# Optimization experiments

Measured on AMD Instinct MI355X. Metric: run time of the kernel, lower is better.

## Reference

```python
import jax, jax.numpy as jnp
import numpy as np


def setup_inputs() -> dict:
    key = jax.random.key(0)
    kx, ka = jax.random.split(key)
    B, N, D = 8, 4096, 32
    x = jax.random.normal(kx, (B, N, D), dtype=jnp.float32)
    # adjacency-like nonnegative weights (dense branch of GsumLayer)
    a = jax.random.uniform(ka, (B, N, N), dtype=jnp.float32)
    return {"x": x, "a": a}


def reference(x, a):
    # GsumLayer dense branch: out[b] = a[b] @ x[b]  -> [B, N, D]
    return jnp.einsum('bnm,bmd->bnd', a, x)
```

## Files before the change

### kernel.cpp

```cpp
#include <hip/hip_runtime.h>


#define GN 4096
#define GD 32
#define GB 8
#define BKC 256
#define NCH (GN / BKC)
#define NT 512
#define NW 8
#define TILE_N 128

typedef float f32x4 __attribute__((ext_vector_type(4)));
typedef short s16x8 __attribute__((ext_vector_type(8)));

__global__ __launch_bounds__(256, 4) void xprep(
    const float* __restrict__ x,
    unsigned short* __restrict__ xth,
    unsigned short* __restrict__ xtl)
{
    const int t  = threadIdx.x;
    const int b  = blockIdx.x >> 5;
    const int kc = blockIdx.x & 31;
    const int d  = t & 31;
    const int kb = t >> 5;
    const int k0 = kc * 128 + kb * 16;
    const float* xb = x + (long long)b * GN * GD;

    __attribute__((aligned(16))) unsigned short hi[16];
    __attribute__((aligned(16))) unsigned short lo[16];
    #pragma unroll
    for (int j = 0; j < 16; ++j) {
        float f = xb[(long long)(k0 + j) * GD + d];
        unsigned u  = __float_as_uint(f);
        unsigned hb = (u + 0x8000u) >> 16;
        float hif   = __uint_as_float(hb << 16);
        hi[j] = (unsigned short)hb;
        lo[j] = (unsigned short)((__float_as_uint(f - hif) + 0x8000u) >> 16);
    }
    long long ob = ((long long)(b * GD + d)) * GN + k0;
    *(s16x8*)(xth + ob)     = *(const s16x8*)&hi[0];
    *(s16x8*)(xth + ob + 8) = *(const s16x8*)&hi[8];
    *(s16x8*)(xtl + ob)     = *(const s16x8*)&lo[0];
    *(s16x8*)(xtl + ob + 8) = *(const s16x8*)&lo[8];
}

__global__ __launch_bounds__(NT, 2) void gsum_mfma(
    const float* __restrict__ a,
    const unsigned short* __restrict__ xth,
    const unsigned short* __restrict__ xtl,
    float* __restrict__ out)
{
    __shared__ float As[NW][16][BKC];

    const int t  = threadIdx.x;
    const int w  = t >> 6;
    const int l  = t & 63;
    const int m  = l & 15;
    const int kg = l >> 4;
    const int m7 = m & 7;

    const int b    = blockIdx.x >> 5;
    const int tile = blockIdx.x & 31;
    const int n0   = tile * TILE_N + w * 16;

    const float* Ab = a + ((long long)b * GN + n0) * GN;
    const unsigned short* xh0p = xth + (long long)(b * GD + m) * GN;
    const unsigned short* xh1p = xh0p + 16 * GN;
    const unsigned short* xl0p = xtl + (long long)(b * GD + m) * GN;
    const unsigned short* xl1p = xl0p + 16 * GN;
    const int kfo = kg * 8;

    float* lds = &As[w][0][0];

    f32x4 acc0 = {0.f, 0.f, 0.f, 0.f};
    f32x4 acc1 = {0.f, 0.f, 0.f, 0.f};
    s16x8 xf[8][4];
    f32x4 st[16];

    auto STAGE = [&](int c) {
        const float* p = Ab + c * BKC + l * 4;
        #pragma unroll
        for (int r = 0; r < 16; ++r)
            st[r] = *(const f32x4*)(p + (long long)r * GN);
    };
    auto DSWRITE = [&]() {
        #pragma unroll
        for (int r = 0; r < 16; ++r)
            *(f32x4*)(lds + r * BKC + ((l ^ (r & 7)) * 4)) = st[r];
    };
    auto FRAGS = [&](int c) {
        #pragma unroll
        for (int s = 0; s < 8; ++s) {
            const long long k = (long long)c * BKC + s * 32 + kfo;
            xf[s][0] = *(const s16x8*)(xh0p + k);
            xf[s][1] = *(const s16x8*)(xh1p + k);
            xf[s][2] = *(const s16x8*)(xl0p + k);
            xf[s][3] = *(const s16x8*)(xl1p + k);
        }
    };
    auto COMPUTE = [&]() {
        #pragma unroll
        for (int s = 0; s < 8; ++s) {
            const int g0 = (((s * 8 + kg * 2)     ^ m7) * 4);
            const int g1 = (((s * 8 + kg * 2 + 1) ^ m7) * 4);
            f32x4 fa = *(const f32x4*)(lds + m * BKC + g0);
            f32x4 fb = *(const f32x4*)(lds + m * BKC + g1);
            s16x8 ahi, alo;
            #pragma unroll
            for (int e = 0; e < 4; ++e) {
                {
                    unsigned u  = __float_as_uint(fa[e]);
                    unsigned hb = (u + 0x8000u) >> 16;
                    ahi[e] = (short)hb;
                    float hif = __uint_as_float(hb << 16);
                    alo[e] = (short)((__float_as_uint(fa[e] - hif) + 0x8000u) >> 16);
                }
                {
                    unsigned u  = __float_as_uint(fb[e]);
                    unsigned hb = (u + 0x8000u) >> 16;
                    ahi[4 + e] = (short)hb;
                    float hif = __uint_as_float(hb << 16);
                    alo[4 + e] = (short)((__float_as_uint(fb[e] - hif) + 0x8000u) >> 16);
                }
            }
            acc0 = __builtin_amdgcn_mfma_f32_16x16x32_bf16(ahi, xf[s][0], acc0, 0, 0, 0);
            acc1 = __builtin_amdgcn_mfma_f32_16x16x32_bf16(ahi, xf[s][1], acc1, 0, 0, 0);
            acc0 = __builtin_amdgcn_mfma_f32_16x16x32_bf16(alo, xf[s][0], acc0, 0, 0, 0);
            acc1 = __builtin_amdgcn_mfma_f32_16x16x32_bf16(alo, xf[s][1], acc1, 0, 0, 0);
            acc0 = __builtin_amdgcn_mfma_f32_16x16x32_bf16(ahi, xf[s][2], acc0, 0, 0, 0);
            acc1 = __builtin_amdgcn_mfma_f32_16x16x32_bf16(ahi, xf[s][3], acc1, 0, 0, 0);
        }
    };

    STAGE(0);
    DSWRITE();
    FRAGS(0);
    __builtin_amdgcn_sched_barrier(0);
    STAGE(1);
    __builtin_amdgcn_sched_barrier(0);

    for (int c = 0; c < NCH; ++c) {
        COMPUTE();
        __builtin_amdgcn_sched_barrier(0);
        if (c + 1 < NCH) {
            DSWRITE();
            __builtin_amdgcn_sched_barrier(0);
            FRAGS(c + 1);
            __builtin_amdgcn_sched_barrier(0);
            if (c + 2 < NCH) {
                STAGE(c + 2);
                __builtin_amdgcn_sched_barrier(0);
            }
        }
    }

    float* Ob = out + ((long long)b * GN + n0) * GD;
    #pragma unroll
    for (int j = 0; j < 4; ++j) {
        Ob[(kg * 4 + j) * GD + m]      = acc0[j];
        Ob[(kg * 4 + j) * GD + 16 + m] = acc1[j];
    }
}

extern "C" void kernel_launch(void* const* d_in, const int* in_sizes, int n_in,
                              void* d_out, int out_size, void* d_ws, size_t ws_size,
                              hipStream_t stream) {
    const float* x = (const float*)d_in[0];
    const float* a = (const float*)d_in[1];
    float* out = (float*)d_out;

    unsigned short* xth = (unsigned short*)d_ws;
    unsigned short* xtl = xth + (long long)GB * GD * GN;

    xprep<<<dim3(GB * 32), dim3(256), 0, stream>>>(x, xth, xtl);
    gsum_mfma<<<dim3(GB * (GN / TILE_N)), dim3(NT), 0, stream>>>(a, xth, xtl, out);
}
```

Before: 741.5 us.

## Stream A fragments directly from global memory, bypassing LDS staging

Replaces the LDS-staged pipeline with direct per-lane global loads of A rows into MFMA fragments, software-pipelined 4 steps ahead for A and 2 steps ahead for X. The MFMA operands are swapped so that A supplies the B-side fragment, which lets each lane load 8 contiguous k values from its own row and makes output stores contiguous. Tiles shrink to 64 rows with 256 threads, and a block-index swizzle spreads batches across the grid. The aim is to remove LDS write/read traffic and the register-heavy 16-row staging. In exchange, each lane issues 32-byte row-strided global loads, which may coalesce less well than the earlier full-row 1 KB staging loads.

```diff
diff --git a/kernel.cpp b/kernel.cpp
--- a/kernel.cpp
+++ b/kernel.cpp
@@ -4,11 +4,9 @@
 #define GN 4096
 #define GD 32
 #define GB 8
-#define BKC 256
-#define NCH (GN / BKC)
-#define NT 512
-#define NW 8
-#define TILE_N 128
+#define NCH 16
+#define TILE_N 64
+#define NT 256
 
 typedef float f32x4 __attribute__((ext_vector_type(4)));
 typedef short s16x8 __attribute__((ext_vector_type(8)));
@@ -44,121 +42,111 @@
     *(s16x8*)(xtl + ob + 8) = *(const s16x8*)&lo[8];
 }
 
-__global__ __launch_bounds__(NT, 2) void gsum_mfma(
+__global__ __launch_bounds__(NT, 2) void gsum_stream(
     const float* __restrict__ a,
     const unsigned short* __restrict__ xth,
     const unsigned short* __restrict__ xtl,
     float* __restrict__ out)
 {
-    __shared__ float As[NW][16][BKC];
-
     const int t  = threadIdx.x;
     const int w  = t >> 6;
     const int l  = t & 63;
     const int m  = l & 15;
     const int kg = l >> 4;
-    const int m7 = m & 7;
 
-    const int b    = blockIdx.x >> 5;
-    const int tile = blockIdx.x & 31;
+    const int bid  = blockIdx.x;
+    const int swz  = (bid & 7) * 64 + (bid >> 3);
+    const int b    = swz >> 6;
+    const int tile = swz & 63;
     const int n0   = tile * TILE_N + w * 16;
 
-    const float* Ab = a + ((long long)b * GN + n0) * GN;
-    const unsigned short* xh0p = xth + (long long)(b * GD + m) * GN;
+    const float* arow = a + ((long long)b * GN + n0 + m) * GN + kg * 8;
+    const unsigned short* xh0p = xth + (long long)(b * GD + m) * GN + kg * 8;
     const unsigned short* xh1p = xh0p + 16 * GN;
-    const unsigned short* xl0p = xtl + (long long)(b * GD + m) * GN;
+    const unsigned short* xl0p = xtl + (long long)(b * GD + m) * GN + kg * 8;
     const unsigned short* xl1p = xl0p + 16 * GN;
-    const int kfo = kg * 8;
-
-    float* lds = &As[w][0][0];
 
     f32x4 acc0 = {0.f, 0.f, 0.f, 0.f};
     f32x4 acc1 = {0.f, 0.f, 0.f, 0.f};
-    s16x8 xf[8][4];
-    f32x4 st[16];
+    f32x4 pa[4][2];
+    s16x8 xf[2][4];
 
-    auto STAGE = [&](int c) {
-        const float* p = Ab + c * BKC + l * 4;
-        #pragma unroll
-        for (int r = 0; r < 16; ++r)
-            st[r] = *(const f32x4*)(p + (long long)r * GN);
-    };
-    auto DSWRITE = [&]() {
-        #pragma unroll
-        for (int r = 0; r < 16; ++r)
-            *(f32x4*)(lds + r * BKC + ((l ^ (r & 7)) * 4)) = st[r];
-    };
-    auto FRAGS = [&](int c) {
+    #pragma unroll
+    for (int g = 0; g < 4; ++g) {
+        pa[g][0] = *(const f32x4*)(arow + g * 32);
+        pa[g][1] = *(const f32x4*)(arow + g * 32 + 4);
+    }
+    #pragma unroll
+    for (int g = 0; g < 2; ++g) {
+        xf[g][0] = *(const s16x8*)(xh0p + g * 32);
+        xf[g][1] = *(const s16x8*)(xh1p + g * 32);
+        xf[g][2] = *(const s16x8*)(xl0p + g * 32);
+        xf[g][3] = *(const s16x8*)(xl1p + g * 32);
+    }
+
+#define STEP_BODY(S, REFILL_A, REFILL_X)                                        \
+    {                                                                           \
+        f32x4 a0 = pa[(S) & 3][0], a1 = pa[(S) & 3][1];                         \
+        s16x8 vh0 = xf[(S) & 1][0], vh1 = xf[(S) & 1][1];                       \
+        s16x8 vl0 = xf[(S) & 1][2], vl1 = xf[(S) & 1][3];                       \
+        if (REFILL_A) {                                                         \
+            const int ga = c * 8 + (S) + 4;                                     \
+            pa[(S) & 3][0] = *(const f32x4*)(arow + ga * 32);                   \
+            pa[(S) & 3][1] = *(const f32x4*)(arow + ga * 32 + 4);               \
+        }                                                                       \
+        if (REFILL_X) {                                                         \
+            const int gx = c * 8 + (S) + 2;                                     \
+            xf[(S) & 1][0] = *(const s16x8*)(xh0p + gx * 32);                   \
+            xf[(S) & 1][1] = *(const s16x8*)(xh1p + gx * 32);                   \
+            xf[(S) & 1][2] = *(const s16x8*)(xl0p + gx * 32);                   \
+            xf[(S) & 1][3] = *(const s16x8*)(xl1p + gx * 32);                   \
+        }                                                                       \
+        s16x8 ahi, alo;                                                         \
+        _Pragma("unroll")                                                       \
+        for (int e = 0; e < 4; ++e) {                                           \
+            {                                                                   \
+                unsigned u  = __float_as_uint(a0[e]);                           \
+                unsigned hb = (u + 0x8000u) >> 16;                              \
+                ahi[e] = (short)hb;                                             \
+                float hif = __uint_as_float(hb << 16);                          \
+                alo[e] = (short)((__float_as_uint(a0[e] - hif) + 0x8000u) >> 16); \
+            }                                                                   \
+            {                                                                   \
+                unsigned u  = __float_as_uint(a1[e]);                           \
+                unsigned hb = (u + 0x8000u) >> 16;                              \
+                ahi[4 + e] = (short)hb;                                         \
+                float hif = __uint_as_float(hb << 16);                          \
+                alo[4 + e] = (short)((__float_as_uint(a1[e] - hif) + 0x8000u) >> 16); \
+            }                                                                   \
+        }                                                                       \
+        acc0 = __builtin_amdgcn_mfma_f32_16x16x32_bf16(vh0, ahi, acc0, 0, 0, 0); \
+        acc1 = __builtin_amdgcn_mfma_f32_16x16x32_bf16(vh1, ahi, acc1, 0, 0, 0); \
+        acc0 = __builtin_amdgcn_mfma_f32_16x16x32_bf16(vl0, ahi, acc0, 0, 0, 0); \
+        acc1 = __builtin_amdgcn_mfma_f32_16x16x32_bf16(vl1, ahi, acc1, 0, 0, 0); \
+        acc0 = __builtin_amdgcn_mfma_f32_16x16x32_bf16(vh0, alo, acc0, 0, 0, 0); \
+        acc1 = __builtin_amdgcn_mfma_f32_16x16x32_bf16(vh1, alo, acc1, 0, 0, 0); \
+    }
+
+    for (int c = 0; c < NCH - 1; ++c) {
         #pragma unroll
         for (int s = 0; s < 8; ++s) {
-            const long long k = (long long)c * BKC + s * 32 + kfo;
-            xf[s][0] = *(const s16x8*)(xh0p + k);
-            xf[s][1] = *(const s16x8*)(xh1p + k);
-            xf[s][2] = *(const s16x8*)(xl0p + k);
-            xf[s][3] = *(const s16x8*)(xl1p + k);
+            STEP_BODY(s, true, true)
         }
-    };
-    auto COMPUTE = [&]() {
+    }
+    {
+        const int c = NCH - 1;
         #pragma unroll
         for (int s = 0; s < 8; ++s) {
-            const int g0 = (((s * 8 + kg * 2)     ^ m7) * 4);
-            const int g1 = (((s * 8 + kg * 2 + 1) ^ m7) * 4);
-            f32x4 fa = *(const f32x4*)(lds + m * BKC + g0);
-            f32x4 fb = *(const f32x4*)(lds + m * BKC + g1);
-            s16x8 ahi, alo;
-            #pragma unroll
-            for (int e = 0; e < 4; ++e) {
-                {
-                    unsigned u  = __float_as_uint(fa[e]);
-                    unsigned hb = (u + 0x8000u) >> 16;
-                    ahi[e] = (short)hb;
-                    float hif = __uint_as_float(hb << 16);
-                    alo[e] = (short)((__float_as_uint(fa[e] - hif) + 0x8000u) >> 16);
-                }
-                {
-                    unsigned u  = __float_as_uint(fb[e]);
-                    unsigned hb = (u + 0x8000u) >> 16;
-                    ahi[4 + e] = (short)hb;
-                    float hif = __uint_as_float(hb << 16);
-                    alo[4 + e] = (short)((__float_as_uint(fb[e] - hif) + 0x8000u) >> 16);
-                }
-            }
-            acc0 = __builtin_amdgcn_mfma_f32_16x16x32_bf16(ahi, xf[s][0], acc0, 0, 0, 0);
-            acc1 = __builtin_amdgcn_mfma_f32_16x16x32_bf16(ahi, xf[s][1], acc1, 0, 0, 0);
-            acc0 = __builtin_amdgcn_mfma_f32_16x16x32_bf16(alo, xf[s][0], acc0, 0, 0, 0);
-            acc1 = __builtin_amdgcn_mfma_f32_16x16x32_bf16(alo, xf[s][1], acc1, 0, 0, 0);
-            acc0 = __builtin_amdgcn_mfma_f32_16x16x32_bf16(ahi, xf[s][2], acc0, 0, 0, 0);
-            acc1 = __builtin_amdgcn_mfma_f32_16x16x32_bf16(ahi, xf[s][3], acc1, 0, 0, 0);
-        }
-    };
-
-    STAGE(0);
-    DSWRITE();
-    FRAGS(0);
-    __builtin_amdgcn_sched_barrier(0);
-    STAGE(1);
-    __builtin_amdgcn_sched_barrier(0);
-
-    for (int c = 0; c < NCH; ++c) {
-        COMPUTE();
-        __builtin_amdgcn_sched_barrier(0);
-        if (c + 1 < NCH) {
-            DSWRITE();
-            __builtin_amdgcn_sched_barrier(0);
-            FRAGS(c + 1);
-            __builtin_amdgcn_sched_barrier(0);
-            if (c + 2 < NCH) {
-                STAGE(c + 2);
-                __builtin_amdgcn_sched_barrier(0);
-            }
+            STEP_BODY(s, (s < 4), (s < 6))
         }
     }
+#undef STEP_BODY
 
-    float* Ob = out + ((long long)b * GN + n0) * GD;
+    float* Ob = out + ((long long)b * GN + n0 + m) * GD + kg * 4;
     #pragma unroll
     for (int j = 0; j < 4; ++j) {
-        Ob[(kg * 4 + j) * GD + m]      = acc0[j];
-        Ob[(kg * 4 + j) * GD + 16 + m] = acc1[j];
+        Ob[j]      = acc0[j];
+        Ob[16 + j] = acc1[j];
     }
 }
 
@@ -173,5 +161,5 @@
     unsigned short* xtl = xth + (long long)GB * GD * GN;
 
     xprep<<<dim3(GB * 32), dim3(256), 0, stream>>>(x, xth, xtl);
-    gsum_mfma<<<dim3(GB * (GN / TILE_N)), dim3(NT), 0, stream>>>(a, xth, xtl, out);
+    gsum_stream<<<dim3(GB * (GN / TILE_N)), dim3(NT), 0, stream>>>(a, xth, xtl, out);
 }
```

New measurement: 742.5 us. Within noise of the previous version (+0.1%).
